# Kernel tuning notes

Measured on AMD Instinct MI355X. Metric: run time of the kernel, lower is better.

Reference implementation:

```python
import jax, jax.numpy as jnp
import numpy as np

N, D, T = 4096, 512, 4096
TEMPERATURE = 0.07
MARGIN = 0.5
CONT_WEIGHT = 1.0
TRIP_WEIGHT = 0.3
EPS = 1e-8        # eps in the log / denominator (matches torch code)
PD_EPS = 1e-6     # F.pairwise_distance default eps added to the difference


def setup_inputs() -> dict:
    key = jax.random.key(0)
    k1, k2, k3 = jax.random.split(key, 3)
    embeddings = jax.random.normal(k1, (N, D), dtype=jnp.float32)
    labels = jax.random.randint(k2, (N,), 0, 256)            # ~16 positives per place
    triplets = jax.random.randint(k3, (T, 3), 0, N)          # (anchor, pos, neg) indices
    return {"embeddings": embeddings, "labels": labels, "triplets": triplets}


def reference(embeddings, labels, triplets):
    # ---- MultiPositiveContrastiveLoss ----
    # F.cosine_similarity normalizes each row with eps=1e-8 on the norm.
    norms = jnp.linalg.norm(embeddings, axis=1, keepdims=True)
    n_emb = embeddings / jnp.maximum(norms, EPS)
    sim = (n_emb @ n_emb.T) / TEMPERATURE                    # [N, N]

    pos_mask = (labels[:, None] == labels[None, :]).astype(embeddings.dtype)
    pos_mask = pos_mask * (1.0 - jnp.eye(sim.shape[0], dtype=embeddings.dtype))

    exp_sim = jnp.exp(sim)
    pos_sum = (exp_sim * pos_mask).sum(axis=1)
    total_sum = exp_sim.sum(axis=1)
    loss = -jnp.log(pos_sum / (total_sum + EPS) + EPS)

    valid = pos_mask.sum(axis=1) > 0
    cnt = valid.sum()
    cont_loss = jnp.where(
        cnt > 0,
        jnp.where(valid, loss, 0.0).sum() / jnp.maximum(cnt, 1).astype(loss.dtype),
        jnp.zeros((), loss.dtype),
    )

    # ---- TripletLoss, vectorized over all triplets (replaces Python loop) ----
    a = embeddings[triplets[:, 0]]   # [T, D]
    p = embeddings[triplets[:, 1]]
    ng = embeddings[triplets[:, 2]]
    pos_dist = jnp.linalg.norm(a - p + PD_EPS, axis=1)
    neg_dist = jnp.linalg.norm(a - ng + PD_EPS, axis=1)
    trip_loss = jnp.maximum(pos_dist - neg_dist + MARGIN, 0.0).mean()

    total = CONT_WEIGHT * cont_loss + TRIP_WEIGHT * trip_loss
    return (total, cont_loss, trip_loss)
```

## Files before the change

kernel.cpp:

```cpp
#include <hip/hip_runtime.h>

#define NN 4096
#define DD 512
#define TT 4096

typedef __bf16 bf16x8 __attribute__((ext_vector_type(8)));
typedef float f32x4 __attribute__((ext_vector_type(4)));

constexpr float INV_TEMP = 1.0f / 0.07f;

#define AS1(p) ((__attribute__((address_space(1))) const void*)(p))
#define AS3(p) ((__attribute__((address_space(3))) void*)(p))

__global__ __launch_bounds__(256) void k_normtrip(const float* __restrict__ emb,
                                                  const int* __restrict__ trip,
                                                  __bf16* __restrict__ nemb,
                                                  float* __restrict__ tl) {
    int wave = threadIdx.x >> 6, lane = threadIdx.x & 63;
    if (blockIdx.x < NN / 4) {
        int row = blockIdx.x * 4 + wave;
        const float4* src = (const float4*)(emb + (size_t)row * DD);
        float4 x0 = src[lane * 2 + 0];
        float4 x1 = src[lane * 2 + 1];
        float ss = x0.x * x0.x + x0.y * x0.y + x0.z * x0.z + x0.w * x0.w +
                   x1.x * x1.x + x1.y * x1.y + x1.z * x1.z + x1.w * x1.w;
        #pragma unroll
        for (int m = 1; m < 64; m <<= 1) ss += __shfl_xor(ss, m, 64);
        float inv = 1.0f / fmaxf(sqrtf(ss), 1e-8f);
        bf16x8 v;
        v[0] = (__bf16)(x0.x * inv); v[1] = (__bf16)(x0.y * inv);
        v[2] = (__bf16)(x0.z * inv); v[3] = (__bf16)(x0.w * inv);
        v[4] = (__bf16)(x1.x * inv); v[5] = (__bf16)(x1.y * inv);
        v[6] = (__bf16)(x1.z * inv); v[7] = (__bf16)(x1.w * inv);
        *(bf16x8*)(nemb + (size_t)row * DD + lane * 8) = v;
    } else {
        int t = (blockIdx.x - NN / 4) * 4 + wave;
        int ia = trip[t * 3 + 0], ip = trip[t * 3 + 1], ig = trip[t * 3 + 2];
        const float4* pa = (const float4*)(emb + (size_t)ia * DD);
        const float4* pp = (const float4*)(emb + (size_t)ip * DD);
        const float4* pn = (const float4*)(emb + (size_t)ig * DD);
        float d1 = 0.0f, d2 = 0.0f;
        #pragma unroll
        for (int j = 0; j < 2; ++j) {
            float4 a = pa[lane * 2 + j];
            float4 p = pp[lane * 2 + j];
            float4 n = pn[lane * 2 + j];
            float dx;
            dx = a.x - p.x + 1e-6f; d1 += dx * dx;
            dx = a.y - p.y + 1e-6f; d1 += dx * dx;
            dx = a.z - p.z + 1e-6f; d1 += dx * dx;
            dx = a.w - p.w + 1e-6f; d1 += dx * dx;
            dx = a.x - n.x + 1e-6f; d2 += dx * dx;
            dx = a.y - n.y + 1e-6f; d2 += dx * dx;
            dx = a.z - n.z + 1e-6f; d2 += dx * dx;
            dx = a.w - n.w + 1e-6f; d2 += dx * dx;
        }
        #pragma unroll
        for (int m = 1; m < 64; m <<= 1) {
            d1 += __shfl_xor(d1, m, 64);
            d2 += __shfl_xor(d2, m, 64);
        }
        if (lane == 0) tl[t] = fmaxf(sqrtf(d1) - sqrtf(d2) + 0.5f, 0.0f);
    }
}

__global__ __launch_bounds__(256) void k_contrast(const __bf16* __restrict__ nemb,
                                                  const int* __restrict__ labels,
                                                  float* __restrict__ posP,
                                                  float* __restrict__ totP,
                                                  float* __restrict__ cntP) {
    __shared__ __attribute__((aligned(16))) __bf16 aSm[64 * 32];
    __shared__ __attribute__((aligned(16))) __bf16 bSm[128 * 32];
    __shared__ int rlab[64];
    __shared__ int clab[128];

    int tid = threadIdx.x;
    int lane = tid & 63, wave = tid >> 6;
    int wc = wave;
    int l15 = lane & 15, quad = lane >> 4;

    int idx = blockIdx.y;
    int half = blockIdx.x;
    int cb = (int)((sqrtf(8.0f * (float)idx + 1.0f) - 1.0f) * 0.5f);
    while ((cb + 1) * (cb + 2) / 2 <= idx) ++cb;
    while (cb * (cb + 1) / 2 > idx) --cb;
    int rb = idx - cb * (cb + 1) / 2;
    int row0 = rb * 128 + half * 64;
    int col0 = cb * 128;
    bool offd = (rb != cb);

    if (tid < 64)       rlab[tid] = labels[row0 + tid];
    else if (tid < 192) clab[tid - 64] = labels[col0 + tid - 64];

    f32x4 acc[4][2];
    #pragma unroll
    for (int r = 0; r < 4; ++r)
        #pragma unroll
        for (int c = 0; c < 2; ++c) {
            f32x4 z = {0.0f, 0.0f, 0.0f, 0.0f};
            acc[r][c] = z;
        }

    const __bf16* gA = nemb + (size_t)(row0 + (tid >> 2)) * DD + (tid & 3) * 8;
    const __bf16* gB = nemb + (size_t)(col0 + (tid >> 2)) * DD + (tid & 3) * 8;

    for (int kt = 0; kt < 16; ++kt) {
        int kb = kt * 32;
        __syncthreads();
        __builtin_amdgcn_global_load_lds(AS1(gA + kb),                   AS3(aSm + tid * 8),         16, 0, 0);
        __builtin_amdgcn_global_load_lds(AS1(gB + kb),                   AS3(bSm + tid * 8),         16, 0, 0);
        __builtin_amdgcn_global_load_lds(AS1(gB + (size_t)64 * DD + kb), AS3(bSm + (tid + 256) * 8), 16, 0, 0);
        __syncthreads();

        bf16x8 af[4], bfr[2];
        #pragma unroll
        for (int r = 0; r < 4; ++r)
            af[r] = *(const bf16x8*)(aSm + (r * 16 + l15) * 32 + quad * 8);
        #pragma unroll
        for (int c = 0; c < 2; ++c)
            bfr[c] = *(const bf16x8*)(bSm + (wc * 32 + c * 16 + l15) * 32 + quad * 8);
        #pragma unroll
        for (int r = 0; r < 4; ++r)
            #pragma unroll
            for (int c = 0; c < 2; ++c)
                acc[r][c] = __builtin_amdgcn_mfma_f32_16x16x32_bf16(af[r], bfr[c], acc[r][c], 0, 0, 0);
    }

    int cl[2];
    #pragma unroll
    for (int c = 0; c < 2; ++c) cl[c] = clab[wc * 32 + c * 16 + l15];

    float tT[2] = {0, 0}, pT[2] = {0, 0}, cT[2] = {0, 0};
    int rslotbase = (cb - rb) * 4 + wc;

    #pragma unroll
    for (int r = 0; r < 4; ++r) {
        float tv[4] = {0, 0, 0, 0}, pv[4] = {0, 0, 0, 0}, cv[4] = {0, 0, 0, 0};
        int gibase = row0 + r * 16 + quad * 4;
        int rl[4];
        #pragma unroll
        for (int v = 0; v < 4; ++v) rl[v] = rlab[r * 16 + quad * 4 + v];
        #pragma unroll
        for (int c = 0; c < 2; ++c) {
            int gj = col0 + wc * 32 + c * 16 + l15;
            #pragma unroll
            for (int v = 0; v < 4; ++v) {
                float e = __expf(acc[r][c][v] * INV_TEMP);
                bool match = (rl[v] == cl[c]) && ((gibase + v) != gj);
                float me = match ? e : 0.0f;
                float mc = match ? 1.0f : 0.0f;
                tv[v] += e;  pv[v] += me;  cv[v] += mc;
                tT[c] += e;  pT[c] += me;  cT[c] += mc;
            }
        }
        #pragma unroll
        for (int m = 1; m < 16; m <<= 1) {
            #pragma unroll
            for (int v = 0; v < 4; ++v) {
                tv[v] += __shfl_xor(tv[v], m, 64);
                pv[v] += __shfl_xor(pv[v], m, 64);
                cv[v] += __shfl_xor(cv[v], m, 64);
            }
        }
        if (l15 == 0) {
            #pragma unroll
            for (int v = 0; v < 4; ++v) {
                int gr = gibase + v;
                int oidx = gr * 128 + rslotbase;
                posP[oidx] = pv[v];
                totP[oidx] = tv[v];
                cntP[oidx] = cv[v];
            }
        }
    }

    if (offd) {
        #pragma unroll
        for (int m = 16; m < 64; m <<= 1) {
            #pragma unroll
            for (int c = 0; c < 2; ++c) {
                tT[c] += __shfl_xor(tT[c], m, 64);
                pT[c] += __shfl_xor(pT[c], m, 64);
                cT[c] += __shfl_xor(cT[c], m, 64);
            }
        }
        if (quad == 0) {
            int mslot = 4 * (32 - cb) + rb * 2 + half;
            #pragma unroll
            for (int c = 0; c < 2; ++c) {
                int gj = col0 + wc * 32 + c * 16 + l15;
                int oidx = gj * 128 + mslot;
                posP[oidx] = pT[c];
                totP[oidx] = tT[c];
                cntP[oidx] = cT[c];
            }
        }
    }
}

__global__ __launch_bounds__(256) void k_rowloss(const float* __restrict__ posP,
                                                 const float* __restrict__ totP,
                                                 const float* __restrict__ cntP,
                                                 float* __restrict__ rloss,
                                                 float* __restrict__ rvalid) {
    int wave = threadIdx.x >> 6, lane = threadIdx.x & 63;
    int row = blockIdx.x * 4 + wave;
    int used = 128 - 2 * (row >> 7);
    float p = posP[row * 128 + lane];
    float t = totP[row * 128 + lane];
    float c = cntP[row * 128 + lane];
    if (64 + lane < used) {
        p += posP[row * 128 + 64 + lane];
        t += totP[row * 128 + 64 + lane];
        c += cntP[row * 128 + 64 + lane];
    }
    #pragma unroll
    for (int m = 1; m < 64; m <<= 1) {
        p += __shfl_xor(p, m, 64);
        t += __shfl_xor(t, m, 64);
        c += __shfl_xor(c, m, 64);
    }
    if (lane == 0) {
        float loss = -logf(p / (t + 1e-8f) + 1e-8f);
        bool valid = c > 0.0f;
        rloss[row] = valid ? loss : 0.0f;
        rvalid[row] = valid ? 1.0f : 0.0f;
    }
}

__global__ __launch_bounds__(256) void k_final(const float* __restrict__ rloss,
                                               const float* __restrict__ rvalid,
                                               const float* __restrict__ tl,
                                               float* __restrict__ out) {
    int tid = threadIdx.x;
    float sl = 0.0f, sv = 0.0f, st = 0.0f;
    for (int i = tid; i < NN; i += 256) {
        sl += rloss[i];
        sv += rvalid[i];
        st += tl[i];
    }
    #pragma unroll
    for (int m = 1; m < 64; m <<= 1) {
        sl += __shfl_xor(sl, m, 64);
        sv += __shfl_xor(sv, m, 64);
        st += __shfl_xor(st, m, 64);
    }
    __shared__ float red[3][4];
    int lane = tid & 63, wave = tid >> 6;
    if (lane == 0) { red[0][wave] = sl; red[1][wave] = sv; red[2][wave] = st; }
    __syncthreads();
    if (tid == 0) {
        float SL = red[0][0] + red[0][1] + red[0][2] + red[0][3];
        float SV = red[1][0] + red[1][1] + red[1][2] + red[1][3];
        float ST = red[2][0] + red[2][1] + red[2][2] + red[2][3];
        float cont = (SV > 0.0f) ? (SL / SV) : 0.0f;
        float trip = ST * (1.0f / (float)TT);
        out[0] = cont + 0.3f * trip;
        out[1] = cont;
        out[2] = trip;
    }
}

extern "C" void kernel_launch(void* const* d_in, const int* in_sizes, int n_in,
                              void* d_out, int out_size, void* d_ws, size_t ws_size,
                              hipStream_t stream) {
    const float* emb = (const float*)d_in[0];
    const int* labels = (const int*)d_in[1];
    const int* trips = (const int*)d_in[2];
    float* out = (float*)d_out;
    char* ws = (char*)d_ws;

    __bf16* nemb  = (__bf16*)(ws);
    float* posP   = (float*)(ws + 4194304);
    float* totP   = (float*)(ws + 6291456);
    float* cntP   = (float*)(ws + 8388608);
    float* rloss  = (float*)(ws + 10485760);
    float* rvalid = (float*)(ws + 10502144);
    float* tl     = (float*)(ws + 10518528);

    k_normtrip<<<NN / 4 + TT / 4, 256, 0, stream>>>(emb, trips, nemb, tl);
    k_contrast<<<dim3(2, 528), 256, 0, stream>>>(nemb, labels, posP, totP, cntP);
    k_rowloss<<<NN / 4, 256, 0, stream>>>(posP, totP, cntP, rloss, rvalid);
    k_final<<<1, 256, 0, stream>>>(rloss, rvalid, tl, out);
}
```

Measured before the change: 112.8 us.

## Double-buffer LDS tiles in contrast GEMM and pre-reduce row partials across waves

The contrast kernel now prefetches the next K-slice into a second LDS buffer while the current slice feeds the MFMAs, so each iteration needs one barrier instead of two. Row-wise partial sums from the four waves are combined in shared memory before they are written, which halves the partial slots per row from 128 to 64. The workspace offsets and the row-loss reduction are updated to match the new slot layout. In exchange, LDS use roughly doubles, and the overlap relies on the end-of-iteration barrier also waiting for the async global-to-LDS loads.

```diff
diff --git a/kernel.cpp b/kernel.cpp
--- a/kernel.cpp
+++ b/kernel.cpp
@@ -69,8 +69,9 @@
                                                   float* __restrict__ posP,
                                                   float* __restrict__ totP,
                                                   float* __restrict__ cntP) {
-    __shared__ __attribute__((aligned(16))) __bf16 aSm[64 * 32];
-    __shared__ __attribute__((aligned(16))) __bf16 bSm[128 * 32];
+    __shared__ __attribute__((aligned(16))) __bf16 aSm[2][64 * 32];
+    __shared__ __attribute__((aligned(16))) __bf16 bSm[2][128 * 32];
+    __shared__ float sred[4][64][3];
     __shared__ int rlab[64];
     __shared__ int clab[128];
 
@@ -104,26 +105,34 @@
     const __bf16* gA = nemb + (size_t)(row0 + (tid >> 2)) * DD + (tid & 3) * 8;
     const __bf16* gB = nemb + (size_t)(col0 + (tid >> 2)) * DD + (tid & 3) * 8;
 
+    __builtin_amdgcn_global_load_lds(AS1(gA),                   AS3(&aSm[0][0] + tid * 8),         16, 0, 0);
+    __builtin_amdgcn_global_load_lds(AS1(gB),                   AS3(&bSm[0][0] + tid * 8),         16, 0, 0);
+    __builtin_amdgcn_global_load_lds(AS1(gB + (size_t)64 * DD), AS3(&bSm[0][0] + (tid + 256) * 8), 16, 0, 0);
+    __syncthreads();
+
     for (int kt = 0; kt < 16; ++kt) {
-        int kb = kt * 32;
-        __syncthreads();
-        __builtin_amdgcn_global_load_lds(AS1(gA + kb),                   AS3(aSm + tid * 8),         16, 0, 0);
-        __builtin_amdgcn_global_load_lds(AS1(gB + kb),                   AS3(bSm + tid * 8),         16, 0, 0);
-        __builtin_amdgcn_global_load_lds(AS1(gB + (size_t)64 * DD + kb), AS3(bSm + (tid + 256) * 8), 16, 0, 0);
-        __syncthreads();
+        int cur = kt & 1, nxt = cur ^ 1;
+        if (kt < 15) {
+            int kb = (kt + 1) * 32;
+            __builtin_amdgcn_global_load_lds(AS1(gA + kb),                   AS3(&aSm[nxt][0] + tid * 8),         16, 0, 0);
+            __builtin_amdgcn_global_load_lds(AS1(gB + kb),                   AS3(&bSm[nxt][0] + tid * 8),         16, 0, 0);
+            __builtin_amdgcn_global_load_lds(AS1(gB + (size_t)64 * DD + kb), AS3(&bSm[nxt][0] + (tid + 256) * 8), 16, 0, 0);
+        }
 
         bf16x8 af[4], bfr[2];
         #pragma unroll
         for (int r = 0; r < 4; ++r)
-            af[r] = *(const bf16x8*)(aSm + (r * 16 + l15) * 32 + quad * 8);
+            af[r] = *(const bf16x8*)(&aSm[cur][0] + (r * 16 + l15) * 32 + quad * 8);
         #pragma unroll
         for (int c = 0; c < 2; ++c)
-            bfr[c] = *(const bf16x8*)(bSm + (wc * 32 + c * 16 + l15) * 32 + quad * 8);
+            bfr[c] = *(const bf16x8*)(&bSm[cur][0] + (wc * 32 + c * 16 + l15) * 32 + quad * 8);
         #pragma unroll
         for (int r = 0; r < 4; ++r)
             #pragma unroll
             for (int c = 0; c < 2; ++c)
                 acc[r][c] = __builtin_amdgcn_mfma_f32_16x16x32_bf16(af[r], bfr[c], acc[r][c], 0, 0, 0);
+
+        __syncthreads();
     }
 
     int cl[2];
@@ -131,7 +140,6 @@
     for (int c = 0; c < 2; ++c) cl[c] = clab[wc * 32 + c * 16 + l15];
 
     float tT[2] = {0, 0}, pT[2] = {0, 0}, cT[2] = {0, 0};
-    int rslotbase = (cb - rb) * 4 + wc;
 
     #pragma unroll
     for (int r = 0; r < 4; ++r) {
@@ -165,13 +173,27 @@
         if (l15 == 0) {
             #pragma unroll
             for (int v = 0; v < 4; ++v) {
-                int gr = gibase + v;
-                int oidx = gr * 128 + rslotbase;
-                posP[oidx] = pv[v];
-                totP[oidx] = tv[v];
-                cntP[oidx] = cv[v];
-            }
-        }
+                int lr = r * 16 + quad * 4 + v;
+                sred[wave][lr][0] = tv[v];
+                sred[wave][lr][1] = pv[v];
+                sred[wave][lr][2] = cv[v];
+            }
+        }
+    }
+    __syncthreads();
+
+    if (tid < 64) {
+        float t = 0.0f, p = 0.0f, c = 0.0f;
+        #pragma unroll
+        for (int w = 0; w < 4; ++w) {
+            t += sred[w][tid][0];
+            p += sred[w][tid][1];
+            c += sred[w][tid][2];
+        }
+        int oidx = (row0 + tid) * 64 + (cb - rb);
+        totP[oidx] = t;
+        posP[oidx] = p;
+        cntP[oidx] = c;
     }
 
     if (offd) {
@@ -185,11 +207,11 @@
             }
         }
         if (quad == 0) {
-            int mslot = 4 * (32 - cb) + rb * 2 + half;
+            int mslot = (32 - cb) + rb * 2 + half;
             #pragma unroll
             for (int c = 0; c < 2; ++c) {
                 int gj = col0 + wc * 32 + c * 16 + l15;
-                int oidx = gj * 128 + mslot;
+                int oidx = gj * 64 + mslot;
                 posP[oidx] = pT[c];
                 totP[oidx] = tT[c];
                 cntP[oidx] = cT[c];
@@ -205,14 +227,12 @@
                                                  float* __restrict__ rvalid) {
     int wave = threadIdx.x >> 6, lane = threadIdx.x & 63;
     int row = blockIdx.x * 4 + wave;
-    int used = 128 - 2 * (row >> 7);
-    float p = posP[row * 128 + lane];
-    float t = totP[row * 128 + lane];
-    float c = cntP[row * 128 + lane];
-    if (64 + lane < used) {
-        p += posP[row * 128 + 64 + lane];
-        t += totP[row * 128 + 64 + lane];
-        c += cntP[row * 128 + 64 + lane];
+    int used = 32 + (row >> 7);
+    float p = 0.0f, t = 0.0f, c = 0.0f;
+    if (lane < used) {
+        p = posP[row * 64 + lane];
+        t = totP[row * 64 + lane];
+        c = cntP[row * 64 + lane];
     }
     #pragma unroll
     for (int m = 1; m < 64; m <<= 1) {
@@ -272,11 +292,11 @@
 
     __bf16* nemb  = (__bf16*)(ws);
     float* posP   = (float*)(ws + 4194304);
-    float* totP   = (float*)(ws + 6291456);
-    float* cntP   = (float*)(ws + 8388608);
-    float* rloss  = (float*)(ws + 10485760);
-    float* rvalid = (float*)(ws + 10502144);
-    float* tl     = (float*)(ws + 10518528);
+    float* totP   = (float*)(ws + 5242880);
+    float* cntP   = (float*)(ws + 6291456);
+    float* rloss  = (float*)(ws + 7340032);
+    float* rvalid = (float*)(ws + 7356416);
+    float* tl     = (float*)(ws + 7372800);
 
     k_normtrip<<<NN / 4 + TT / 4, 256, 0, stream>>>(emb, trips, nemb, tl);
     k_contrast<<<dim3(2, 528), 256, 0, stream>>>(nemb, labels, posP, totP, cntP);
```

Measured after the change: 113.4 us. About the same (+0.5%).
